# Kernel optimization log

Measured on AMD Instinct MI355X. Metric: run time of the kernel, lower is better.

## Reference

```python
import jax, jax.numpy as jnp
import numpy as np

B, N, D_IN, D_OUT = 16, 2048, 128, 128

def setup_inputs() -> dict:
    key = jax.random.key(0)
    ks = jax.random.split(key, 8)
    x = jax.random.normal(ks[0], (B, N, D_IN), dtype=jnp.float32)
    adj = jax.random.randint(ks[1], (N, N), 0, 2).astype(jnp.float32)
    # Conv1d(kernel_size=1) weights, PyTorch default uniform init scale
    s_emb = 1.0 / np.sqrt(D_IN)
    W_emb = jax.random.uniform(ks[2], (D_OUT, D_IN), jnp.float32, -s_emb, s_emb)
    b_emb = jax.random.uniform(ks[3], (D_OUT,), jnp.float32, -s_emb, s_emb)
    s_qk = 1.0 / np.sqrt(D_OUT)
    w_q = jax.random.uniform(ks[4], (D_OUT,), jnp.float32, -s_qk, s_qk)
    b_q = jax.random.uniform(ks[5], (1,), jnp.float32, -s_qk, s_qk)
    w_k = jax.random.uniform(ks[6], (D_OUT,), jnp.float32, -s_qk, s_qk)
    b_k = jax.random.uniform(ks[7], (1,), jnp.float32, -s_qk, s_qk)
    return {"x": x, "adj": adj, "W_emb": W_emb, "b_emb": b_emb,
            "w_q": w_q, "b_q": b_q, "w_k": w_k, "b_k": b_k}

def reference(x, adj, W_emb, b_emb, w_q, b_q, w_k, b_k):
    # emb_conv: 1x1 conv over node dim == per-node linear  [B,N,D_out]
    seq_fts = jnp.einsum('bni,oi->bno', x, W_emb) + b_emb
    # q_conv / k_conv: project to scalar per node  [B,N]
    q = jnp.einsum('bnd,d->bn', seq_fts, w_q) + b_q  # f_1_t squeezed
    k = jnp.einsum('bnd,d->bn', seq_fts, w_k) + b_k  # f_2_t squeezed
    # f[b,i,j] = f_1_t[b,0,j] + f_2_t^T[b,i,0] = q[b,j] + k[b,i]
    f = k[:, :, None] + q[:, None, :]                 # [B,N,N]
    f = jax.nn.leaky_relu(adj[None, :, :] * f, negative_slope=0.01)
    coefs = jax.nn.softmax(f, axis=1)                 # softmax over dim=1 (rows)
    vals = jnp.einsum('bij,bjd->bid', coefs, seq_fts)  # [B,N,D_out]
    return vals
```

## Files before the change

kernel.cpp:

```cpp
#include <hip/hip_runtime.h>
#include <hip/hip_bf16.h>
#include <stdint.h>

#define B_ 16
#define N_ 2048
#define D_ 128

typedef __bf16 bf16_t;
typedef bf16_t bf16x8 __attribute__((ext_vector_type(8)));
typedef float f32x4 __attribute__((ext_vector_type(4)));

__global__ __launch_bounds__(256) void k_pack_adj(const float* __restrict__ adj,
                                                  unsigned int* __restrict__ bits) {
    int t = blockIdx.x * 256 + threadIdx.x;
    float v = adj[t];
    unsigned long long m = __ballot(v > 0.5f);
    if ((t & 63) == 0) {
        int i = t >> 11;
        int j = t & 2047;
        bits[i * 64 + (j >> 5)]     = (unsigned int)m;
        bits[i * 64 + (j >> 5) + 1] = (unsigned int)(m >> 32);
    }
}

__global__ __launch_bounds__(256, 2) void k_emb(const float* __restrict__ x,
                                                const float* __restrict__ W,
                                                const float* __restrict__ be,
                                                const float* __restrict__ wq,
                                                const float* __restrict__ bq,
                                                const float* __restrict__ wk,
                                                const float* __restrict__ bk,
                                                bf16_t* __restrict__ Pb,
                                                float* __restrict__ qa, float* __restrict__ ka,
                                                float* __restrict__ Eq, float* __restrict__ eqs,
                                                float* __restrict__ Ek, float* __restrict__ eks,
                                                float* __restrict__ denom) {
    __shared__ float xs[32][68];
    __shared__ float ws[32][132];
    __shared__ float qs[64], ks[64];
    int b  = blockIdx.y;
    int n0 = blockIdx.x * 64;
    int tid = threadIdx.x;
    int tx = tid & 15, ty = tid >> 4;
    if (tid < 64) { qs[tid] = 0.f; ks[tid] = 0.f; }

    float acc[4][8] = {};
    f32x4 xr[2], wr[4];

    auto loadregs = [&](int kc) {
#pragma unroll
        for (int s = 0; s < 2; ++s) {
            int p = tid + 256 * s;
            int n = p >> 3, kq = p & 7;
            xr[s] = *(const f32x4*)(x + ((size_t)(b * N_ + n0 + n)) * D_ + kc * 32 + kq * 4);
        }
#pragma unroll
        for (int s = 0; s < 4; ++s) {
            int p = tid + 256 * s;
            int d = p >> 3, kq = p & 7;
            wr[s] = *(const f32x4*)(W + (size_t)d * D_ + kc * 32 + kq * 4);
        }
    };
    auto writelds = [&]() {
#pragma unroll
        for (int s = 0; s < 2; ++s) {
            int p = tid + 256 * s;
            int n = p >> 3, kq = p & 7;
#pragma unroll
            for (int u = 0; u < 4; ++u) xs[kq * 4 + u][n] = xr[s][u];
        }
#pragma unroll
        for (int s = 0; s < 4; ++s) {
            int p = tid + 256 * s;
            int d = p >> 3, kq = p & 7;
#pragma unroll
            for (int u = 0; u < 4; ++u) ws[kq * 4 + u][d] = wr[s][u];
        }
    };

    loadregs(0);
    for (int kc = 0; kc < 4; ++kc) {
        writelds();
        __syncthreads();
        if (kc < 3) loadregs(kc + 1);
#pragma unroll 4
        for (int k = 0; k < 32; ++k) {
            f32x4 xv  = *(const f32x4*)&xs[k][tx * 4];
            f32x4 wv0 = *(const f32x4*)&ws[k][ty * 8];
            f32x4 wv1 = *(const f32x4*)&ws[k][ty * 8 + 4];
#pragma unroll
            for (int i = 0; i < 4; ++i)
#pragma unroll
                for (int j = 0; j < 8; ++j)
                    acc[i][j] += xv[i] * ((j < 4) ? wv0[j] : wv1[j - 4]);
        }
        __syncthreads();
    }

    float qp[4] = {}, kp[4] = {};
#pragma unroll
    for (int j = 0; j < 8; ++j) {
        int d = ty * 8 + j;
        float bj  = be[d];
        float wqj = wq[d];
        float wkj = wk[d];
        f32x4 o;
        bf16_t ob[4];
#pragma unroll
        for (int i = 0; i < 4; ++i) {
            o[i] = acc[i][j] + bj;
            qp[i] += o[i] * wqj;
            kp[i] += o[i] * wkj;
            ob[i] = (bf16_t)o[i];
        }
        *(uint2*)(Pb + ((size_t)b * D_ + d) * N_ + n0 + tx * 4) = *(uint2*)ob;
    }
#pragma unroll
    for (int i = 0; i < 4; ++i) {
        atomicAdd(&qs[tx * 4 + i], qp[i]);
        atomicAdd(&ks[tx * 4 + i], kp[i]);
    }
    __syncthreads();
    if (tid < 64) {
        int idx = b * N_ + n0 + tid;
        float aq = qs[tid] + bq[0];
        float ak = ks[tid] + bk[0];
        qa[idx] = aq;          ka[idx] = ak;
        Eq[idx] = expf(aq);    eqs[idx] = expf(0.01f * aq);
        Ek[idx] = expf(ak);    eks[idx] = expf(0.01f * ak);
        denom[idx] = 0.f;
    }
}

__global__ __launch_bounds__(256) void k_denom(const unsigned int* __restrict__ bits,
                                               const float* __restrict__ qa,
                                               const float* __restrict__ ka,
                                               const float* __restrict__ Eq,
                                               const float* __restrict__ eqs,
                                               const float* __restrict__ Ek,
                                               const float* __restrict__ eks,
                                               float* __restrict__ denom) {
    int jt  = blockIdx.x;
    int b   = blockIdx.y;
    int seg = blockIdx.z;
    int j = jt * 256 + threadIdx.x;
    float qj  = qa[b * N_ + j];
    float Eqj = Eq[b * N_ + j];
    float eqj = eqs[b * N_ + j];
    int shift = j & 31;
    int wid   = j >> 5;
    float acc = 0.f;
    int i0 = seg * 256;
#pragma unroll 16
    for (int i = i0; i < i0 + 256; ++i) {
        float kk  = ka[b * N_ + i];
        float Ekk = Ek[b * N_ + i];
        float ekk = eks[b * N_ + i];
        unsigned int w = bits[i * 64 + wid];
        float z  = kk + qj;
        float f1 = z > 0.f ? Ekk : ekk;
        float f2 = z > 0.f ? Eqj : eqj;
        float v  = f1 * f2;
        acc += ((w >> shift) & 1u) ? v : 1.0f;
    }
    atomicAdd(&denom[b * N_ + j], acc);
}

__global__ __launch_bounds__(256) void k_post(const float* __restrict__ denom,
                                              const float* __restrict__ Eq,
                                              const float* __restrict__ eqs,
                                              float* __restrict__ rd,
                                              float* __restrict__ Eqr,
                                              float* __restrict__ eqr) {
    int t = blockIdx.x * 256 + threadIdx.x;
    float r = 1.0f / denom[t];
    rd[t]  = r;
    Eqr[t] = Eq[t] * r;
    eqr[t] = eqs[t] * r;
}

__global__ __launch_bounds__(256, 2) void k_attn(const float* __restrict__ qa,
                                                 const float* __restrict__ ka,
                                                 const float* __restrict__ Ek,
                                                 const float* __restrict__ eks,
                                                 const float* __restrict__ rd,
                                                 const float* __restrict__ Eqr,
                                                 const float* __restrict__ eqr,
                                                 const unsigned int* __restrict__ bits,
                                                 const bf16_t* __restrict__ Pb,
                                                 float* __restrict__ out) {
    __shared__ __align__(16) bf16_t ldsB[2][128 * 64];
    __shared__ __align__(16) bf16_t ldsA[4 * 2 * 64 * 8];
    int n     = blockIdx.x;
    int xcd   = n & 7;
    int slot  = n >> 3;
    int b     = xcd * 2 + (slot >> 5);
    int ibase = (slot & 31) * 64;
    int tid   = threadIdx.x;
    int w     = tid >> 6;
    int lane  = tid & 63;
    int m16   = lane & 15;
    int quad  = lane >> 4;
    int ig    = w & 1;
    int dg    = w >> 1;

    int iA = ibase + (2 * ig) * 16 + m16;
    int iB = iA + 16;
    float mkR0 = -ka[b * N_ + iA], mkR1 = -ka[b * N_ + iB];
    float EkR0 = Ek[b * N_ + iA],  EkR1 = Ek[b * N_ + iB];
    float ekR0 = eks[b * N_ + iA], ekR1 = eks[b * N_ + iB];
    const unsigned int* brA = bits + (size_t)iA * 64;
    const unsigned int* brB = bits + (size_t)iB * 64;
    const float* qp  = qa  + b * N_;
    const float* Erp = Eqr + b * N_;
    const float* erp = eqr + b * N_;
    const float* rdp = rd  + b * N_;
    const bf16_t* PtB = Pb + (size_t)b * D_ * N_;

    f32x4 acc[2][4];
#pragma unroll
    for (int c = 0; c < 2; ++c)
#pragma unroll
        for (int nt = 0; nt < 4; ++nt) acc[c][nt] = (f32x4){0.f, 0.f, 0.f, 0.f};

    f32x4 qv4[2][2], Er4[2][2], er4[2][2], rd4[2][2];
    unsigned int mA[2], mB[2];

    auto ldj = [&](int par, int jb) {
        int j0 = jb + dg * 32 + quad * 8;
        qv4[par][0] = *(const f32x4*)(qp  + j0);
        qv4[par][1] = *(const f32x4*)(qp  + j0 + 4);
        Er4[par][0] = *(const f32x4*)(Erp + j0);
        Er4[par][1] = *(const f32x4*)(Erp + j0 + 4);
        er4[par][0] = *(const f32x4*)(erp + j0);
        er4[par][1] = *(const f32x4*)(erp + j0 + 4);
        rd4[par][0] = *(const f32x4*)(rdp + j0);
        rd4[par][1] = *(const f32x4*)(rdp + j0 + 4);
        mA[par] = brA[(jb >> 5) + dg];
        mB[par] = brB[(jb >> 5) + dg];
    };

    auto stage = [&](int bufi, int jb) {
#pragma unroll
        for (int t = 0; t < 4; ++t) {
            int off = t * 4096 + tid * 16;
            int d   = off >> 7;
            int g   = ((off & 127) >> 4) ^ (d & 7);
            const bf16_t* gp = PtB + (size_t)d * N_ + jb + g * 8;
            __builtin_amdgcn_global_load_lds(
                (const __attribute__((address_space(1))) void*)gp,
                (__attribute__((address_space(3))) void*)((char*)(&ldsB[bufi][0]) + off),
                16, 0, 0);
        }
    };

    auto agen = [&](int par, bf16x8& afA, bf16x8& afB) {
#pragma unroll
        for (int t = 0; t < 8; ++t) {
            float qv = (t < 4) ? qv4[par][0][t] : qv4[par][1][t - 4];
            float Er = (t < 4) ? Er4[par][0][t] : Er4[par][1][t - 4];
            float er = (t < 4) ? er4[par][0][t] : er4[par][1][t - 4];
            float rj = (t < 4) ? rd4[par][0][t] : rd4[par][1][t - 4];
            int bit = quad * 8 + t;
            {
                bool c = qv > mkR0;
                float v = (c ? EkR0 : ekR0) * (c ? Er : er);
                afA[t] = (bf16_t)(((mA[par] >> bit) & 1u) ? v : rj);
            }
            {
                bool c = qv > mkR1;
                float v = (c ? EkR1 : ekR1) * (c ? Er : er);
                afB[t] = (bf16_t)(((mB[par] >> bit) & 1u) ? v : rj);
            }
        }
        *(bf16x8*)((char*)ldsA + ((((2 * ig + 0) * 2 + dg) * 64 + lane) * 16)) = afA;
        *(bf16x8*)((char*)ldsA + ((((2 * ig + 1) * 2 + dg) * 64 + lane) * 16)) = afB;
    };

    auto mfma_phase = [&](int buf, const bf16x8& afA, const bf16x8& afB) {
        {
            int cph = ((dg * 4 + quad) ^ (m16 & 7)) * 8;
#pragma unroll
            for (int nt = 0; nt < 4; ++nt) {
                int d = dg * 64 + nt * 16 + m16;
                bf16x8 bf = *(const bf16x8*)&ldsB[buf][d * 64 + cph];
                acc[0][nt] = __builtin_amdgcn_mfma_f32_16x16x32_bf16(afA, bf, acc[0][nt], 0, 0, 0);
                acc[1][nt] = __builtin_amdgcn_mfma_f32_16x16x32_bf16(afB, bf, acc[1][nt], 0, 0, 0);
            }
        }
        {
            int oh = 1 - dg;
            bf16x8 a0 = *(const bf16x8*)((char*)ldsA + ((((2 * ig + 0) * 2 + oh) * 64 + lane) * 16));
            bf16x8 a1 = *(const bf16x8*)((char*)ldsA + ((((2 * ig + 1) * 2 + oh) * 64 + lane) * 16));
            int cph = ((oh * 4 + quad) ^ (m16 & 7)) * 8;
#pragma unroll
            for (int nt = 0; nt < 4; ++nt) {
                int d = dg * 64 + nt * 16 + m16;
                bf16x8 bf = *(const bf16x8*)&ldsB[buf][d * 64 + cph];
                acc[0][nt] = __builtin_amdgcn_mfma_f32_16x16x32_bf16(a0, bf, acc[0][nt], 0, 0, 0);
                acc[1][nt] = __builtin_amdgcn_mfma_f32_16x16x32_bf16(a1, bf, acc[1][nt], 0, 0, 0);
            }
        }
    };

    stage(0, 0);
    ldj(0, 0);
    int buf = 0;
#pragma unroll 1
    for (int s2 = 0; s2 < 15; ++s2) {
#pragma unroll
        for (int par = 0; par < 2; ++par) {
            int jb = (s2 * 2 + par) * 64;
            ldj(par ^ 1, jb + 64);
            stage(buf ^ 1, jb + 64);

            bf16x8 afA, afB;
            agen(par, afA, afB);
            asm volatile("s_waitcnt vmcnt(14) lgkmcnt(0)" ::: "memory");
            __builtin_amdgcn_s_barrier();

            __builtin_amdgcn_s_setprio(1);
            mfma_phase(buf, afA, afB);
            __builtin_amdgcn_s_setprio(0);

            asm volatile("s_waitcnt lgkmcnt(0)" ::: "memory");
            __builtin_amdgcn_s_barrier();
            buf ^= 1;
        }
    }
    {
        ldj(1, 31 * 64);
        stage(buf ^ 1, 31 * 64);
        bf16x8 afA, afB;
        agen(0, afA, afB);
        asm volatile("s_waitcnt vmcnt(14) lgkmcnt(0)" ::: "memory");
        __builtin_amdgcn_s_barrier();
        __builtin_amdgcn_s_setprio(1);
        mfma_phase(buf, afA, afB);
        __builtin_amdgcn_s_setprio(0);
        asm volatile("s_waitcnt lgkmcnt(0)" ::: "memory");
        __builtin_amdgcn_s_barrier();
        buf ^= 1;
    }
    {
        bf16x8 afA, afB;
        agen(1, afA, afB);
        asm volatile("s_waitcnt vmcnt(0) lgkmcnt(0)" ::: "memory");
        __builtin_amdgcn_s_barrier();
        __builtin_amdgcn_s_setprio(1);
        mfma_phase(buf, afA, afB);
        __builtin_amdgcn_s_setprio(0);
    }

#pragma unroll
    for (int c = 0; c < 2; ++c) {
        int irow = ibase + (2 * ig + c) * 16 + quad * 4;
#pragma unroll
        for (int nt = 0; nt < 4; ++nt) {
            int d = dg * 64 + nt * 16 + m16;
#pragma unroll
            for (int r = 0; r < 4; ++r)
                out[((size_t)b * N_ + irow + r) * D_ + d] = acc[c][nt][r];
        }
    }
}

extern "C" void kernel_launch(void* const* d_in, const int* in_sizes, int n_in,
                              void* d_out, int out_size, void* d_ws, size_t ws_size,
                              hipStream_t stream) {
    const float* x   = (const float*)d_in[0];
    const float* adj = (const float*)d_in[1];
    const float* W   = (const float*)d_in[2];
    const float* be  = (const float*)d_in[3];
    const float* wq  = (const float*)d_in[4];
    const float* bq  = (const float*)d_in[5];
    const float* wk  = (const float*)d_in[6];
    const float* bk  = (const float*)d_in[7];
    float* out = (float*)d_out;

    char* ws = (char*)d_ws;
    size_t off = 0;
    bf16_t* Pb = (bf16_t*)(ws + off); off += (size_t)B_ * D_ * N_ * 2;
    float* qa  = (float*)(ws + off);  off += (size_t)B_ * N_ * 4;
    float* ka  = (float*)(ws + off);  off += (size_t)B_ * N_ * 4;
    float* denom = (float*)(ws + off); off += (size_t)B_ * N_ * 4;
    float* Eq  = (float*)(ws + off);  off += (size_t)B_ * N_ * 4;
    float* eqs = (float*)(ws + off);  off += (size_t)B_ * N_ * 4;
    float* Ek  = (float*)(ws + off);  off += (size_t)B_ * N_ * 4;
    float* eks = (float*)(ws + off);  off += (size_t)B_ * N_ * 4;
    float* rd  = (float*)(ws + off);  off += (size_t)B_ * N_ * 4;
    float* Eqr = (float*)(ws + off);  off += (size_t)B_ * N_ * 4;
    float* eqr = (float*)(ws + off);  off += (size_t)B_ * N_ * 4;
    unsigned int* bits = (unsigned int*)(ws + off); off += (size_t)N_ * 64 * 4;

    k_pack_adj<<<N_ * N_ / 256, 256, 0, stream>>>(adj, bits);
    k_emb<<<dim3(N_ / 64, B_), 256, 0, stream>>>(x, W, be, wq, bq, wk, bk,
                                                 Pb, qa, ka, Eq, eqs, Ek, eks, denom);
    k_denom<<<dim3(8, 16, 8), 256, 0, stream>>>(bits, qa, ka, Eq, eqs, Ek, eks, denom);
    k_post<<<B_ * N_ / 256, 256, 0, stream>>>(denom, Eq, eqs, rd, Eqr, eqr);
    k_attn<<<512, 256, 0, stream>>>(qa, ka, Ek, eks, rd, Eqr, eqr,
                                    bits, Pb, out);
}
```

Baseline: 183.1 us.

## Fuse adjacency bit-packing into embedding kernel and fold reciprocal into attention

Adjacency bit-packing moves into the embedding kernel as a grid-strided loop, removing the separate pack launch. The post-processing kernel that computed reciprocal denominators and scaled exponentials is removed; the attention kernel now reads the raw denominators and computes rcp and the products inline. This saves two launches and some global traffic, at the cost of extra VALU work in the attention A-generation and added memory traffic inside the embedding kernel. It also switches to an approximate reciprocal.

```diff
diff --git a/kernel.cpp b/kernel.cpp
--- a/kernel.cpp
+++ b/kernel.cpp
@@ -9,19 +9,6 @@
 typedef __bf16 bf16_t;
 typedef bf16_t bf16x8 __attribute__((ext_vector_type(8)));
 typedef float f32x4 __attribute__((ext_vector_type(4)));
-
-__global__ __launch_bounds__(256) void k_pack_adj(const float* __restrict__ adj,
-                                                  unsigned int* __restrict__ bits) {
-    int t = blockIdx.x * 256 + threadIdx.x;
-    float v = adj[t];
-    unsigned long long m = __ballot(v > 0.5f);
-    if ((t & 63) == 0) {
-        int i = t >> 11;
-        int j = t & 2047;
-        bits[i * 64 + (j >> 5)]     = (unsigned int)m;
-        bits[i * 64 + (j >> 5) + 1] = (unsigned int)(m >> 32);
-    }
-}
 
 __global__ __launch_bounds__(256, 2) void k_emb(const float* __restrict__ x,
                                                 const float* __restrict__ W,
@@ -30,6 +17,8 @@
                                                 const float* __restrict__ bq,
                                                 const float* __restrict__ wk,
                                                 const float* __restrict__ bk,
+                                                const float* __restrict__ adj,
+                                                unsigned int* __restrict__ bits,
                                                 bf16_t* __restrict__ Pb,
                                                 float* __restrict__ qa, float* __restrict__ ka,
                                                 float* __restrict__ Eq, float* __restrict__ eqs,
@@ -43,6 +32,22 @@
     int tid = threadIdx.x;
     int tx = tid & 15, ty = tid >> 4;
     if (tid < 64) { qs[tid] = 0.f; ks[tid] = 0.f; }
+
+    {
+        int base = (blockIdx.y * (N_ / 64) + blockIdx.x) * 256 + tid;
+#pragma unroll 8
+        for (int it = 0; it < (N_ * N_) / (512 * 256); ++it) {
+            int t = base + it * (512 * 256);
+            float v = adj[t];
+            unsigned long long m = __ballot(v > 0.5f);
+            if ((t & 63) == 0) {
+                int i = t >> 11;
+                int j = t & 2047;
+                bits[i * 64 + (j >> 5)]     = (unsigned int)m;
+                bits[i * 64 + (j >> 5) + 1] = (unsigned int)(m >> 32);
+            }
+        }
+    }
 
     float acc[4][8] = {};
     f32x4 xr[2], wr[4];
@@ -166,26 +171,13 @@
     atomicAdd(&denom[b * N_ + j], acc);
 }
 
-__global__ __launch_bounds__(256) void k_post(const float* __restrict__ denom,
-                                              const float* __restrict__ Eq,
-                                              const float* __restrict__ eqs,
-                                              float* __restrict__ rd,
-                                              float* __restrict__ Eqr,
-                                              float* __restrict__ eqr) {
-    int t = blockIdx.x * 256 + threadIdx.x;
-    float r = 1.0f / denom[t];
-    rd[t]  = r;
-    Eqr[t] = Eq[t] * r;
-    eqr[t] = eqs[t] * r;
-}
-
 __global__ __launch_bounds__(256, 2) void k_attn(const float* __restrict__ qa,
                                                  const float* __restrict__ ka,
                                                  const float* __restrict__ Ek,
                                                  const float* __restrict__ eks,
-                                                 const float* __restrict__ rd,
-                                                 const float* __restrict__ Eqr,
-                                                 const float* __restrict__ eqr,
+                                                 const float* __restrict__ denom,
+                                                 const float* __restrict__ Eq,
+                                                 const float* __restrict__ eqs,
                                                  const unsigned int* __restrict__ bits,
                                                  const bf16_t* __restrict__ Pb,
                                                  float* __restrict__ out) {
@@ -211,10 +203,10 @@
     float ekR0 = eks[b * N_ + iA], ekR1 = eks[b * N_ + iB];
     const unsigned int* brA = bits + (size_t)iA * 64;
     const unsigned int* brB = bits + (size_t)iB * 64;
-    const float* qp  = qa  + b * N_;
-    const float* Erp = Eqr + b * N_;
-    const float* erp = eqr + b * N_;
-    const float* rdp = rd  + b * N_;
+    const float* qp  = qa    + b * N_;
+    const float* dnp = denom + b * N_;
+    const float* Eqp = Eq    + b * N_;
+    const float* eqp = eqs   + b * N_;
     const bf16_t* PtB = Pb + (size_t)b * D_ * N_;
 
     f32x4 acc[2][4];
@@ -223,19 +215,19 @@
 #pragma unroll
         for (int nt = 0; nt < 4; ++nt) acc[c][nt] = (f32x4){0.f, 0.f, 0.f, 0.f};
 
-    f32x4 qv4[2][2], Er4[2][2], er4[2][2], rd4[2][2];
+    f32x4 qv4[2][2], dn4[2][2], Eq4[2][2], eq4[2][2];
     unsigned int mA[2], mB[2];
 
     auto ldj = [&](int par, int jb) {
         int j0 = jb + dg * 32 + quad * 8;
         qv4[par][0] = *(const f32x4*)(qp  + j0);
         qv4[par][1] = *(const f32x4*)(qp  + j0 + 4);
-        Er4[par][0] = *(const f32x4*)(Erp + j0);
-        Er4[par][1] = *(const f32x4*)(Erp + j0 + 4);
-        er4[par][0] = *(const f32x4*)(erp + j0);
-        er4[par][1] = *(const f32x4*)(erp + j0 + 4);
-        rd4[par][0] = *(const f32x4*)(rdp + j0);
-        rd4[par][1] = *(const f32x4*)(rdp + j0 + 4);
+        dn4[par][0] = *(const f32x4*)(dnp + j0);
+        dn4[par][1] = *(const f32x4*)(dnp + j0 + 4);
+        Eq4[par][0] = *(const f32x4*)(Eqp + j0);
+        Eq4[par][1] = *(const f32x4*)(Eqp + j0 + 4);
+        eq4[par][0] = *(const f32x4*)(eqp + j0);
+        eq4[par][1] = *(const f32x4*)(eqp + j0 + 4);
         mA[par] = brA[(jb >> 5) + dg];
         mB[par] = brB[(jb >> 5) + dg];
     };
@@ -258,9 +250,12 @@
 #pragma unroll
         for (int t = 0; t < 8; ++t) {
             float qv = (t < 4) ? qv4[par][0][t] : qv4[par][1][t - 4];
-            float Er = (t < 4) ? Er4[par][0][t] : Er4[par][1][t - 4];
-            float er = (t < 4) ? er4[par][0][t] : er4[par][1][t - 4];
-            float rj = (t < 4) ? rd4[par][0][t] : rd4[par][1][t - 4];
+            float dv = (t < 4) ? dn4[par][0][t] : dn4[par][1][t - 4];
+            float Ev = (t < 4) ? Eq4[par][0][t] : Eq4[par][1][t - 4];
+            float ev = (t < 4) ? eq4[par][0][t] : eq4[par][1][t - 4];
+            float rj = __builtin_amdgcn_rcpf(dv);
+            float Er = Ev * rj;
+            float er = ev * rj;
             int bit = quad * 8 + t;
             {
                 bool c = qv > mkR0;
@@ -388,16 +383,12 @@
     float* eqs = (float*)(ws + off);  off += (size_t)B_ * N_ * 4;
     float* Ek  = (float*)(ws + off);  off += (size_t)B_ * N_ * 4;
     float* eks = (float*)(ws + off);  off += (size_t)B_ * N_ * 4;
-    float* rd  = (float*)(ws + off);  off += (size_t)B_ * N_ * 4;
-    float* Eqr = (float*)(ws + off);  off += (size_t)B_ * N_ * 4;
-    float* eqr = (float*)(ws + off);  off += (size_t)B_ * N_ * 4;
     unsigned int* bits = (unsigned int*)(ws + off); off += (size_t)N_ * 64 * 4;
 
-    k_pack_adj<<<N_ * N_ / 256, 256, 0, stream>>>(adj, bits);
     k_emb<<<dim3(N_ / 64, B_), 256, 0, stream>>>(x, W, be, wq, bq, wk, bk,
+                                                 adj, bits,
                                                  Pb, qa, ka, Eq, eqs, Ek, eks, denom);
     k_denom<<<dim3(8, 16, 8), 256, 0, stream>>>(bits, qa, ka, Eq, eqs, Ek, eks, denom);
-    k_post<<<B_ * N_ / 256, 256, 0, stream>>>(denom, Eq, eqs, rd, Eqr, eqr);
-    k_attn<<<512, 256, 0, stream>>>(qa, ka, Ek, eks, rd, Eqr, eqr,
+    k_attn<<<512, 256, 0, stream>>>(qa, ka, Ek, eks, denom, Eq, eqs,
                                     bits, Pb, out);
 }
```

Measured after the change: 186.8 us. 2.1% more time.

## Fuse adjacency packing into embedding and denominator finalize into reduction kernel

Applied to the files above, without the earlier changes.

The adjacency bit-packing pass is folded into the embedding kernel as a grid-stride loop, which removes one launch. The denominator kernel now reduces its 8 row segments in shared memory within a 1024-thread block and computes the reciprocals and scaled exponentials directly. This drops the atomics, the zeroing of the denominator, and the separate post kernel. The risks are heavier embedding blocks and lower occupancy from the large 1024-thread denominator blocks.

```diff
diff --git a/kernel.cpp b/kernel.cpp
--- a/kernel.cpp
+++ b/kernel.cpp
@@ -9,19 +9,6 @@
 typedef __bf16 bf16_t;
 typedef bf16_t bf16x8 __attribute__((ext_vector_type(8)));
 typedef float f32x4 __attribute__((ext_vector_type(4)));
-
-__global__ __launch_bounds__(256) void k_pack_adj(const float* __restrict__ adj,
-                                                  unsigned int* __restrict__ bits) {
-    int t = blockIdx.x * 256 + threadIdx.x;
-    float v = adj[t];
-    unsigned long long m = __ballot(v > 0.5f);
-    if ((t & 63) == 0) {
-        int i = t >> 11;
-        int j = t & 2047;
-        bits[i * 64 + (j >> 5)]     = (unsigned int)m;
-        bits[i * 64 + (j >> 5) + 1] = (unsigned int)(m >> 32);
-    }
-}
 
 __global__ __launch_bounds__(256, 2) void k_emb(const float* __restrict__ x,
                                                 const float* __restrict__ W,
@@ -30,11 +17,12 @@
                                                 const float* __restrict__ bq,
                                                 const float* __restrict__ wk,
                                                 const float* __restrict__ bk,
+                                                const float* __restrict__ adj,
+                                                unsigned int* __restrict__ bits,
                                                 bf16_t* __restrict__ Pb,
                                                 float* __restrict__ qa, float* __restrict__ ka,
                                                 float* __restrict__ Eq, float* __restrict__ eqs,
-                                                float* __restrict__ Ek, float* __restrict__ eks,
-                                                float* __restrict__ denom) {
+                                                float* __restrict__ Ek, float* __restrict__ eks) {
     __shared__ float xs[32][68];
     __shared__ float ws[32][132];
     __shared__ float qs[64], ks[64];
@@ -43,6 +31,22 @@
     int tid = threadIdx.x;
     int tx = tid & 15, ty = tid >> 4;
     if (tid < 64) { qs[tid] = 0.f; ks[tid] = 0.f; }
+
+    {
+        int base = (blockIdx.y * (N_ / 64) + blockIdx.x) * 256 + tid;
+#pragma unroll 8
+        for (int it = 0; it < (N_ * N_) / (512 * 256); ++it) {
+            int t = base + it * (512 * 256);
+            float v = adj[t];
+            unsigned long long m = __ballot(v > 0.5f);
+            if ((t & 63) == 0) {
+                int i = t >> 11;
+                int j = t & 2047;
+                bits[i * 64 + (j >> 5)]     = (unsigned int)m;
+                bits[i * 64 + (j >> 5) + 1] = (unsigned int)(m >> 32);
+            }
+        }
+    }
 
     float acc[4][8] = {};
     f32x4 xr[2], wr[4];
@@ -128,29 +132,33 @@
         qa[idx] = aq;          ka[idx] = ak;
         Eq[idx] = expf(aq);    eqs[idx] = expf(0.01f * aq);
         Ek[idx] = expf(ak);    eks[idx] = expf(0.01f * ak);
-        denom[idx] = 0.f;
     }
 }
 
-__global__ __launch_bounds__(256) void k_denom(const unsigned int* __restrict__ bits,
-                                               const float* __restrict__ qa,
-                                               const float* __restrict__ ka,
-                                               const float* __restrict__ Eq,
-                                               const float* __restrict__ eqs,
-                                               const float* __restrict__ Ek,
-                                               const float* __restrict__ eks,
-                                               float* __restrict__ denom) {
+__global__ __launch_bounds__(1024) void k_denom(const unsigned int* __restrict__ bits,
+                                                const float* __restrict__ qa,
+                                                const float* __restrict__ ka,
+                                                const float* __restrict__ Eq,
+                                                const float* __restrict__ eqs,
+                                                const float* __restrict__ Ek,
+                                                const float* __restrict__ eks,
+                                                float* __restrict__ rd,
+                                                float* __restrict__ Eqr,
+                                                float* __restrict__ eqr) {
+    __shared__ float red[8][128];
     int jt  = blockIdx.x;
     int b   = blockIdx.y;
-    int seg = blockIdx.z;
-    int j = jt * 256 + threadIdx.x;
+    int tid = threadIdx.x;
+    int tj  = tid & 127;
+    int sg  = tid >> 7;
+    int j   = jt * 128 + tj;
     float qj  = qa[b * N_ + j];
     float Eqj = Eq[b * N_ + j];
     float eqj = eqs[b * N_ + j];
     int shift = j & 31;
     int wid   = j >> 5;
     float acc = 0.f;
-    int i0 = seg * 256;
+    int i0 = sg * 256;
 #pragma unroll 16
     for (int i = i0; i < i0 + 256; ++i) {
         float kk  = ka[b * N_ + i];
@@ -160,23 +168,20 @@
         float z  = kk + qj;
         float f1 = z > 0.f ? Ekk : ekk;
         float f2 = z > 0.f ? Eqj : eqj;
-        float v  = f1 * f2;
-        acc += ((w >> shift) & 1u) ? v : 1.0f;
-    }
-    atomicAdd(&denom[b * N_ + j], acc);
-}
-
-__global__ __launch_bounds__(256) void k_post(const float* __restrict__ denom,
-                                              const float* __restrict__ Eq,
-                                              const float* __restrict__ eqs,
-                                              float* __restrict__ rd,
-                                              float* __restrict__ Eqr,
-                                              float* __restrict__ eqr) {
-    int t = blockIdx.x * 256 + threadIdx.x;
-    float r = 1.0f / denom[t];
-    rd[t]  = r;
-    Eqr[t] = Eq[t] * r;
-    eqr[t] = eqs[t] * r;
+        acc += ((w >> shift) & 1u) ? f1 * f2 : 1.0f;
+    }
+    red[sg][tj] = acc;
+    __syncthreads();
+    if (sg == 0) {
+        float den = acc;
+#pragma unroll
+        for (int s = 1; s < 8; ++s) den += red[s][tj];
+        float r = 1.0f / den;
+        int idx = b * N_ + j;
+        rd[idx]  = r;
+        Eqr[idx] = Eqj * r;
+        eqr[idx] = eqj * r;
+    }
 }
 
 __global__ __launch_bounds__(256, 2) void k_attn(const float* __restrict__ qa,
@@ -383,7 +388,6 @@
     bf16_t* Pb = (bf16_t*)(ws + off); off += (size_t)B_ * D_ * N_ * 2;
     float* qa  = (float*)(ws + off);  off += (size_t)B_ * N_ * 4;
     float* ka  = (float*)(ws + off);  off += (size_t)B_ * N_ * 4;
-    float* denom = (float*)(ws + off); off += (size_t)B_ * N_ * 4;
     float* Eq  = (float*)(ws + off);  off += (size_t)B_ * N_ * 4;
     float* eqs = (float*)(ws + off);  off += (size_t)B_ * N_ * 4;
     float* Ek  = (float*)(ws + off);  off += (size_t)B_ * N_ * 4;
@@ -393,11 +397,11 @@
     float* eqr = (float*)(ws + off);  off += (size_t)B_ * N_ * 4;
     unsigned int* bits = (unsigned int*)(ws + off); off += (size_t)N_ * 64 * 4;
 
-    k_pack_adj<<<N_ * N_ / 256, 256, 0, stream>>>(adj, bits);
     k_emb<<<dim3(N_ / 64, B_), 256, 0, stream>>>(x, W, be, wq, bq, wk, bk,
-                                                 Pb, qa, ka, Eq, eqs, Ek, eks, denom);
-    k_denom<<<dim3(8, 16, 8), 256, 0, stream>>>(bits, qa, ka, Eq, eqs, Ek, eks, denom);
-    k_post<<<B_ * N_ / 256, 256, 0, stream>>>(denom, Eq, eqs, rd, Eqr, eqr);
+                                                 adj, bits,
+                                                 Pb, qa, ka, Eq, eqs, Ek, eks);
+    k_denom<<<dim3(16, 16), 1024, 0, stream>>>(bits, qa, ka, Eq, eqs, Ek, eks,
+                                               rd, Eqr, eqr);
     k_attn<<<512, 256, 0, stream>>>(qa, ka, Ek, eks, rd, Eqr, eqr,
                                     bits, Pb, out);
 }
```

Measured after the change: 188.7 us. 3.1% more time.
